# Optimization experiments

Measured on AMD Instinct MI355X. Metric: run time of the kernel, lower is better.

Reference implementation:

```python
import jax, jax.numpy as jnp
import numpy as np

B, S, HID, NH, HD, E, K = 8, 1024, 1024, 16, 64, 8, 2
IDIM = 2 * HD  # expert internal dim
EPS = 1e-5


def layer_norm(x, g, b):
    m = jnp.mean(x, axis=-1, keepdims=True)
    v = jnp.mean(jnp.square(x - m), axis=-1, keepdims=True)
    return (x - m) * jax.lax.rsqrt(v + EPS) * g + b


def setup_inputs() -> dict:
    key = jax.random.key(0)
    ks = jax.random.split(key, 12)
    n = jax.random.normal
    return {
        "queries": n(ks[0], (B, S, HID), jnp.float32),
        "keys": n(ks[1], (B, S, HID), jnp.float32),
        "values": n(ks[2], (B, S, HID), jnp.float32),
        "memorys": n(ks[3], (B, NH, S, HD), jnp.float32),
        "Wq": n(ks[4], (HD, HD), jnp.float32) * 0.02,
        "Wk": n(ks[5], (HD, HD), jnp.float32) * 0.02,
        "Wv": n(ks[6], (HD, HD), jnp.float32) * 0.02,
        "forget_gate": n(ks[7], (HD,), jnp.float32),
        "gate_W": n(ks[8], (E, HD), jnp.float32) * 0.02,
        "gate_b": jnp.zeros((E,), jnp.float32),
        "ln1_g": jnp.ones((E, HD), jnp.float32),
        "ln1_b": jnp.zeros((E, HD), jnp.float32),
        "W1": n(ks[9], (E, IDIM, HD), jnp.float32) * 0.02,
        "ln2_g": jnp.ones((E, IDIM), jnp.float32),
        "ln2_b": jnp.zeros((E, IDIM), jnp.float32),
        "W2": n(ks[10], (E, HD, IDIM), jnp.float32) * 0.02,
        "b2": jnp.zeros((E, HD), jnp.float32),
    }


def reference(queries, keys, values, memorys, Wq, Wk, Wv, forget_gate,
              gate_W, gate_b, ln1_g, ln1_b, W1, ln2_g, ln2_b, W2, b2):
    bsz, seq, _ = queries.shape
    gelu = lambda x: jax.nn.gelu(x, approximate=False)

    # head split: [B,S,HID] -> [B,NH,S,HD]
    q = queries.reshape(bsz, seq, NH, HD).transpose(0, 2, 1, 3)
    k = keys.reshape(bsz, seq, NH, HD).transpose(0, 2, 1, 3)
    v = values.reshape(bsz, seq, NH, HD).transpose(0, 2, 1, 3)

    q_ = q @ Wq.T
    k_ = k @ Wk.T
    v_ = v @ Wv.T

    # gated memory cell
    cell = k_ * v_ + forget_gate * memorys
    current_memorys = (1.0 - forget_gate) * cell + forget_gate * memorys
    cell_values = q_ * current_memorys  # [B,NH,S,HD]

    # token-mixing MoE (per-token, over last dim)
    x = cell_values.reshape(-1, HD)  # [N, HD], N = B*NH*S
    logits = x @ gate_W.T + gate_b  # [N, E]
    topv, topi = jax.lax.top_k(logits, K)  # [N, K]
    # sparse combine weights [N, E] (raw gate values, as in the original)
    w = jnp.sum(jax.nn.one_hot(topi, E, dtype=x.dtype) * topv[..., None], axis=1)

    def expert_fwd(g1, b1, w1, g2, b2_, w2, bias2):
        h = gelu(layer_norm(x, g1, b1)) @ w1.T      # [N, IDIM]
        h = gelu(layer_norm(h, g2, b2_)) @ w2.T + bias2  # [N, HD]
        return h

    all_out = jax.vmap(expert_fwd)(ln1_g, ln1_b, W1, ln2_g, ln2_b, W2, b2)  # [E,N,HD]
    moe = jnp.einsum('ne,end->nd', w, all_out)  # [N, HD]

    token_mixing = moe.reshape(bsz, NH, seq, HD).transpose(0, 2, 1, 3).reshape(bsz, seq, NH * HD)
    return token_mixing, current_memorys
```

## Files before the change

### kernel.cpp

```cpp
#include <hip/hip_runtime.h>
#include <stdint.h>

typedef unsigned short u16;
typedef unsigned int   u32;
typedef unsigned long long u64;
typedef __attribute__((ext_vector_type(8))) short short8;
typedef __attribute__((ext_vector_type(4))) short s16x4;
typedef __attribute__((ext_vector_type(4))) float f32x4;

#define B_    8
#define S_    1024
#define HID_  1024
#define NH_   16
#define HD_   64
#define E_    8
#define IDIM_ 128
#define NTOK  (B_*NH_*S_)

#define CSTRIDE 16

__device__ __forceinline__ float bf2f(u16 u){ return __uint_as_float(((u32)u) << 16); }
__device__ __forceinline__ u16 f2bf(float f){
    u32 u = __float_as_uint(f);
    u32 r = u + 0x7fffu + ((u >> 16) & 1u);
    return (u16)(r >> 16);
}
__device__ __forceinline__ short8 frag8(const float* __restrict__ p){
    float4 a = *(const float4*)p;
    float4 b = *(const float4*)(p + 4);
    short8 r;
    r[0]=(short)f2bf(a.x); r[1]=(short)f2bf(a.y); r[2]=(short)f2bf(a.z); r[3]=(short)f2bf(a.w);
    r[4]=(short)f2bf(b.x); r[5]=(short)f2bf(b.y); r[6]=(short)f2bf(b.z); r[7]=(short)f2bf(b.w);
    return r;
}
__device__ __forceinline__ float gelu_exact(float x){
    return 0.5f * x * (1.0f + erff(x * 0.70710678118654752f));
}
__device__ __forceinline__ float gelu_f(float x){
    float z = 1.5957691216057308f * (x + 0.044715f * x * x * x);
    float e = __expf(z);
    float t = 1.0f - 2.0f / (e + 1.0f);
    return 0.5f * x * (1.0f + t);
}

__global__ void k_zero(u32* c){
    c[threadIdx.x] = 0;
}

__global__ __launch_bounds__(256) void k_prep(
    const float* __restrict__ W1, const float* __restrict__ W2,
    u16* __restrict__ wB1, u16* __restrict__ wB2)
{
    const int i = blockIdx.x*256 + threadIdx.x;
    wB1[i] = f2bf(W1[i]);
    wB2[i] = f2bf(W2[i]);
}

__global__ __launch_bounds__(256,2) void k_mem(
    const float* __restrict__ kin, const float* __restrict__ vin, const float* __restrict__ mem,
    const float* __restrict__ Wk,  const float* __restrict__ Wv,  const float* __restrict__ fg,
    float* __restrict__ cur_out)
{
    const int lane = threadIdx.x & 63;
    const int wid  = threadIdx.x >> 6;
    const int m    = lane & 15;
    const int kg   = lane >> 4;

    const int slab  = blockIdx.x;
    const int chunk = slab & 3, h = (slab >> 2) & 15, b = slab >> 6;
    const int tw    = chunk*256 + wid*64;

    const float* kbase = kin + ((size_t)b*S_)*HID_ + h*64;
    const float* vbase = vin + ((size_t)b*S_)*HID_ + h*64;

    f32x4 accK[4][4], accV[4][4];
    const f32x4 z = {0.f,0.f,0.f,0.f};
    #pragma unroll
    for (int i=0;i<4;i++){ accK[i][0]=z;accK[i][1]=z;accK[i][2]=z;accK[i][3]=z;
                           accV[i][0]=z;accV[i][1]=z;accV[i][2]=z;accV[i][3]=z; }

    #pragma unroll
    for (int kk=0; kk<2; kk++){
        const int k0 = kk*32 + kg*8;
        short8 aF[4], bF[4];
        #pragma unroll
        for (int mt=0; mt<4; mt++) aF[mt] = frag8(kbase + (size_t)(tw + mt*16 + m)*HID_ + k0);
        #pragma unroll
        for (int ct=0; ct<4; ct++) bF[ct] = frag8(Wk + (ct*16 + m)*64 + k0);
        #pragma unroll
        for (int mt=0; mt<4; mt++)
            #pragma unroll
            for (int ct=0; ct<4; ct++)
                accK[mt][ct] = __builtin_amdgcn_mfma_f32_16x16x32_bf16(aF[mt], bF[ct], accK[mt][ct], 0,0,0);
    }
    #pragma unroll
    for (int kk=0; kk<2; kk++){
        const int k0 = kk*32 + kg*8;
        short8 aF[4], bF[4];
        #pragma unroll
        for (int mt=0; mt<4; mt++) aF[mt] = frag8(vbase + (size_t)(tw + mt*16 + m)*HID_ + k0);
        #pragma unroll
        for (int ct=0; ct<4; ct++) bF[ct] = frag8(Wv + (ct*16 + m)*64 + k0);
        #pragma unroll
        for (int mt=0; mt<4; mt++)
            #pragma unroll
            for (int ct=0; ct<4; ct++)
                accV[mt][ct] = __builtin_amdgcn_mfma_f32_16x16x32_bf16(aF[mt], bF[ct], accV[mt][ct], 0,0,0);
    }

    const size_t nb = ((size_t)(b*NH_ + h)) << 10;
    float fgv[4];
    #pragma unroll
    for (int ct=0; ct<4; ct++) fgv[ct] = fg[ct*16 + m];

    #pragma unroll
    for (int mt=0; mt<4; mt++){
        #pragma unroll
        for (int r=0; r<4; r++){
            const int tok = tw + mt*16 + kg*4 + r;
            const size_t rowo = (nb + (size_t)tok)*64;
            #pragma unroll
            for (int ct=0; ct<4; ct++){
                const int d = ct*16 + m;
                const float kd = accK[mt][ct][r];
                const float vd = accV[mt][ct][r];
                const float f  = fgv[ct];
                const float mv = mem[rowo + d];
                const float cell = kd*vd + f*mv;
                cur_out[rowo + d] = (1.0f - f)*cell + f*mv;
            }
        }
    }
}

__global__ __launch_bounds__(256,2) void k_q(
    const float* __restrict__ qin, const float* __restrict__ cur_in, const float* __restrict__ Wq,
    float* __restrict__ out0)
{
    const int lane = threadIdx.x & 63;
    const int wid  = threadIdx.x >> 6;
    const int m    = lane & 15;
    const int kg   = lane >> 4;

    const int slab  = blockIdx.x;
    const int chunk = slab & 3, h = (slab >> 2) & 15, b = slab >> 6;
    const int tw    = chunk*256 + wid*64;

    const float* qbase = qin + ((size_t)b*S_)*HID_ + h*64;

    f32x4 accQ[4][4];
    const f32x4 z = {0.f,0.f,0.f,0.f};
    #pragma unroll
    for (int i=0;i<4;i++){ accQ[i][0]=z;accQ[i][1]=z;accQ[i][2]=z;accQ[i][3]=z; }

    #pragma unroll
    for (int kk=0; kk<2; kk++){
        const int k0 = kk*32 + kg*8;
        short8 aF[4], bF[4];
        #pragma unroll
        for (int mt=0; mt<4; mt++) aF[mt] = frag8(qbase + (size_t)(tw + mt*16 + m)*HID_ + k0);
        #pragma unroll
        for (int ct=0; ct<4; ct++) bF[ct] = frag8(Wq + (ct*16 + m)*64 + k0);
        #pragma unroll
        for (int mt=0; mt<4; mt++)
            #pragma unroll
            for (int ct=0; ct<4; ct++)
                accQ[mt][ct] = __builtin_amdgcn_mfma_f32_16x16x32_bf16(aF[mt], bF[ct], accQ[mt][ct], 0,0,0);
    }

    const size_t nb = ((size_t)(b*NH_ + h)) << 10;
    #pragma unroll
    for (int mt=0; mt<4; mt++){
        #pragma unroll
        for (int r=0; r<4; r++){
            const int tok = tw + mt*16 + kg*4 + r;
            const size_t curo = (nb + (size_t)tok)*64;
            const size_t po   = ((size_t)(b*S_ + tok)*NH_ + h)*64;
            #pragma unroll
            for (int ct=0; ct<4; ct++){
                const int d = ct*16 + m;
                out0[po + d] = accQ[mt][ct][r] * cur_in[curo + d];
            }
        }
    }
}

__global__ __launch_bounds__(256,2) void k_gate(
    const float* __restrict__ x_src, const float* __restrict__ gW, const float* __restrict__ gB,
    uint4* __restrict__ topiv, u32* __restrict__ counts)
{
    __shared__ float sGW[512], sGB[8];
    __shared__ u32 sWc[4][8];
    const int tid = threadIdx.x;
    for (int i = tid; i < 512; i += 256) sGW[i] = gW[i];
    if (tid < 8) sGB[tid] = gB[tid];
    __syncthreads();

    const int n = blockIdx.x*256 + tid;
    const int s = n & (S_-1), h = (n >> 10) & (NH_-1), b = n >> 14;
    const size_t po = ((size_t)(b*S_ + s)*NH_ + h)*64;

    float lg[8];
    #pragma unroll
    for (int e = 0; e < 8; e++) lg[e] = sGB[e];

    for (int dc = 0; dc < 16; dc++){
        float4 x4 = ((const float4*)(x_src + po))[dc];
        float xv[4] = {x4.x, x4.y, x4.z, x4.w};
        #pragma unroll
        for (int i = 0; i < 4; i++){
            const int d = dc*4 + i;
            #pragma unroll
            for (int e = 0; e < 8; e++) lg[e] += sGW[e*64 + d] * xv[i];
        }
    }

    int i1 = 0; float v1 = lg[0];
    #pragma unroll
    for (int e = 1; e < 8; e++){ if (lg[e] > v1){ v1 = lg[e]; i1 = e; } }
    int i2 = -1; float v2 = -3.0e38f;
    #pragma unroll
    for (int e = 0; e < 8; e++){ if (e != i1 && lg[e] > v2){ v2 = lg[e]; i2 = e; } }

    topiv[n] = make_uint4((u32)i1, (u32)i2, __float_as_uint(v1), __float_as_uint(v2));

    const int lane = tid & 63;
    const int w    = tid >> 6;
    #pragma unroll
    for (int e = 0; e < 8; e++){
        u64 m1 = __ballot(i1 == e);
        u64 m2 = __ballot(i2 == e);
        if (lane == 0) sWc[w][e] = (u32)(__popcll(m1) + __popcll(m2));
    }
    __syncthreads();
    if (tid < 8){
        u32 t = sWc[0][tid] + sWc[1][tid] + sWc[2][tid] + sWc[3][tid];
        if (t) atomicAdd(&counts[tid*CSTRIDE], t);
    }
}

__global__ __launch_bounds__(256,2) void k_scatter(
    const uint4* __restrict__ topiv, const u32* __restrict__ counts, u32* __restrict__ cursors,
    u32* __restrict__ bucket, int2* __restrict__ slots)
{
    __shared__ u32 sC1[4][8], sC2[4][8];
    __shared__ u32 sB1[4][8], sB2w[4][8];

    const int tid = threadIdx.x;
    const int n = blockIdx.x*256 + tid;
    uint4 t = topiv[n];
    const int i1 = (int)t.x, i2 = (int)t.y;

    int off[8]; int acc = 0;
    #pragma unroll
    for (int e = 0; e < 8; e++){ off[e] = acc; acc += (int)counts[e*CSTRIDE]; }

    const int s = n & (S_-1), h = (n >> 10) & (NH_-1), b = n >> 14;
    const u32 pos32 = (u32)((b*S_ + s)*NH_ + h);

    const int lane = tid & 63;
    const int w    = tid >> 6;
    const u64 low = (1ull << lane) - 1ull;

    u64 myM1 = 0, myM2 = 0;
    #pragma unroll
    for (int e = 0; e < 8; e++){
        u64 m1 = __ballot(i1 == e);
        u64 m2 = __ballot(i2 == e);
        if (i1 == e) myM1 = m1;
        if (i2 == e) myM2 = m2;
        if (lane == 0){ sC1[w][e] = (u32)__popcll(m1); sC2[w][e] = (u32)__popcll(m2); }
    }
    __syncthreads();

    if (tid < 8){
        const int e = tid;
        u32 tot = 0;
        #pragma unroll
        for (int ww = 0; ww < 4; ww++) tot += sC1[ww][e] + sC2[ww][e];
        u32 base = tot ? atomicAdd(&cursors[e*CSTRIDE], tot) : 0;
        u32 run = base;
        #pragma unroll
        for (int ww = 0; ww < 4; ww++){
            sB1[ww][e] = run; run += sC1[ww][e];
            sB2w[ww][e] = run; run += sC2[ww][e];
        }
    }
    __syncthreads();

    const int slot1 = off[i1] + (int)sB1[w][i1] + (int)__popcll(myM1 & low);
    const int slot2 = off[i2] + (int)sB2w[w][i2] + (int)__popcll(myM2 & low);

    bucket[slot1] = pos32;
    bucket[slot2] = pos32;
    slots[n] = make_int2(slot1, slot2);
}

__global__ __launch_bounds__(256,3) void k_expert_mfma(
    const float* __restrict__ x_src, const u32* __restrict__ bucket, const u32* __restrict__ counts,
    const u16* __restrict__ wB1, const u16* __restrict__ wB2,
    const float* __restrict__ l1g, const float* __restrict__ l1b,
    const float* __restrict__ l2g, const float* __restrict__ l2b,
    const float* __restrict__ b2,  u16* __restrict__ aout)
{
    const int e = blockIdx.x >> 10;
    const int c = blockIdx.x & 1023;
    const int cnt = (int)counts[e*CSTRIDE];
    const int aBase = c * 128;
    if (aBase >= cnt) return;

    int off = 0;
    #pragma unroll
    for (int ee = 0; ee < 8; ee++){ if (ee < e) off += (int)counts[ee*CSTRIDE]; }

    __shared__ __align__(16) u16 sH[4][32*128];
    __shared__ float sL1g[64], sL1b[64], sL2g[128], sL2b[128], sB2[64];

    const int tid = threadIdx.x;
    if (tid < 64){ sL1g[tid] = l1g[e*64+tid]; sL1b[tid] = l1b[e*64+tid]; sB2[tid] = b2[e*64+tid]; }
    else if (tid < 192){ int t = tid - 64; sL2g[t] = l2g[e*128+t]; sL2b[t] = l2b[e*128+t]; }
    __syncthreads();

    const int lane = tid & 63;
    const int w    = tid >> 6;
    const int m    = lane & 15;
    const int kg   = lane >> 4;
    const int tb   = aBase + w*32;
    char* sHw = (char*)(&sH[w][0]);

    int pos[2];
    #pragma unroll
    for (int t = 0; t < 2; t++){
        int a = tb + t*16 + m; if (a > cnt-1) a = cnt-1;
        pos[t] = (int)bucket[off + a];
    }

    short8 aF[2][2];
    #pragma unroll
    for (int t = 0; t < 2; t++){
        const float* rp = x_src + ((size_t)(u32)pos[t] << 6);
        float4 v0 = *(const float4*)(rp + kg*8);
        float4 v1 = *(const float4*)(rp + kg*8 + 4);
        float4 v2 = *(const float4*)(rp + 32 + kg*8);
        float4 v3 = *(const float4*)(rp + 32 + kg*8 + 4);
        float s0 = (v0.x+v0.y+v0.z+v0.w) + (v1.x+v1.y+v1.z+v1.w)
                 + (v2.x+v2.y+v2.z+v2.w) + (v3.x+v3.y+v3.z+v3.w);
        float s1 = (v0.x*v0.x+v0.y*v0.y+v0.z*v0.z+v0.w*v0.w)
                 + (v1.x*v1.x+v1.y*v1.y+v1.z*v1.z+v1.w*v1.w)
                 + (v2.x*v2.x+v2.y*v2.y+v2.z*v2.z+v2.w*v2.w)
                 + (v3.x*v3.x+v3.y*v3.y+v3.z*v3.z+v3.w*v3.w);
        s0 += __shfl_xor(s0, 16); s0 += __shfl_xor(s0, 32);
        s1 += __shfl_xor(s1, 16); s1 += __shfl_xor(s1, 32);
        const float mu = s0 * (1.0f/64.0f);
        const float rs = rsqrtf(s1 * (1.0f/64.0f) - mu*mu + 1e-5f);
        float xv[16] = {v0.x,v0.y,v0.z,v0.w, v1.x,v1.y,v1.z,v1.w,
                        v2.x,v2.y,v2.z,v2.w, v3.x,v3.y,v3.z,v3.w};
        #pragma unroll
        for (int kk = 0; kk < 2; kk++){
            short8 f;
            #pragma unroll
            for (int j = 0; j < 8; j++){
                const int k = kk*32 + kg*8 + j;
                f[j] = (short)f2bf(gelu_f((xv[kk*8+j] - mu)*rs*sL1g[k] + sL1b[k]));
            }
            aF[t][kk] = f;
        }
    }

    const f32x4 z = {0.f,0.f,0.f,0.f};
    f32x4 acc1[2][8];
    #pragma unroll
    for (int t = 0; t < 2; t++)
        #pragma unroll
        for (int ct = 0; ct < 8; ct++) acc1[t][ct] = z;

    const u16* wB1e = wB1 + e*8192;
    #pragma unroll
    for (int kk = 0; kk < 2; kk++){
        const int k0 = kk*32 + kg*8;
        short8 bF[8];
        #pragma unroll
        for (int ct = 0; ct < 8; ct++)
            bF[ct] = *(const short8*)(wB1e + (ct*16 + m)*64 + k0);
        #pragma unroll
        for (int t = 0; t < 2; t++)
            #pragma unroll
            for (int ct = 0; ct < 8; ct++)
                acc1[t][ct] = __builtin_amdgcn_mfma_f32_16x16x32_bf16(aF[t][kk], bF[ct], acc1[t][ct], 0,0,0);
    }

    #pragma unroll
    for (int t = 0; t < 2; t++){
        #pragma unroll
        for (int r = 0; r < 4; r++){
            float p0 = 0.f, p1 = 0.f;
            #pragma unroll
            for (int ct = 0; ct < 8; ct++){ float v = acc1[t][ct][r]; p0 += v; p1 += v*v; }
            #pragma unroll
            for (int msk = 1; msk < 16; msk <<= 1){
                p0 += __shfl_xor(p0, msk);
                p1 += __shfl_xor(p1, msk);
            }
            const float mu = p0 * (1.0f/128.0f);
            const float rs = rsqrtf(p1 * (1.0f/128.0f) - mu*mu + 1e-5f);
            const int row = t*16 + kg*4 + r;
            #pragma unroll
            for (int ct = 0; ct < 8; ct++){
                const int col = ct*16 + m;
                *(u16*)(sHw + (((row<<8) + (col<<1)) ^ ((row&7)<<4)))
                    = f2bf(gelu_f((acc1[t][ct][r] - mu)*rs*sL2g[col] + sL2b[col]));
            }
        }
    }

    f32x4 acc2[2][4];
    #pragma unroll
    for (int t = 0; t < 2; t++)
        #pragma unroll
        for (int ct = 0; ct < 4; ct++) acc2[t][ct] = z;

    const u16* wB2e = wB2 + e*8192;
    #pragma unroll
    for (int kk = 0; kk < 4; kk++){
        const int k0 = kk*32 + kg*8;
        short8 aF2[2], bF2[4];
        #pragma unroll
        for (int t = 0; t < 2; t++){
            const int row = t*16 + m;
            aF2[t] = *(const short8*)(sHw + (((row<<8) + (k0<<1)) ^ ((row&7)<<4)));
        }
        #pragma unroll
        for (int ct = 0; ct < 4; ct++)
            bF2[ct] = *(const short8*)(wB2e + (ct*16 + m)*128 + k0);
        #pragma unroll
        for (int t = 0; t < 2; t++)
            #pragma unroll
            for (int ct = 0; ct < 4; ct++)
                acc2[t][ct] = __builtin_amdgcn_mfma_f32_16x16x32_bf16(aF2[t], bF2[ct], acc2[t][ct], 0,0,0);
    }

    #pragma unroll
    for (int t = 0; t < 2; t++){
        #pragma unroll
        for (int r = 0; r < 4; r++){
            const int row = t*16 + kg*4 + r;
            #pragma unroll
            for (int ct = 0; ct < 4; ct++){
                const int col = ct*16 + m;
                *(u16*)(sHw + (((row<<7) + (col<<1)) ^ ((row&7)<<4)))
                    = f2bf(acc2[t][ct][r] + sB2[col]);
            }
        }
    }

    #pragma unroll
    for (int it = 0; it < 4; it++){
        const int idx = it*64 + lane;
        const int row = idx >> 3, qq = idx & 7;
        if (tb + row < cnt){
            uint4 v = *(const uint4*)(sHw + (((row<<7) + (qq<<4)) ^ ((row&7)<<4)));
            *(uint4*)(aout + ((size_t)(off + tb + row) << 6) + qq*8) = v;
        }
    }
}

__global__ __launch_bounds__(256,2) void k_expert(
    const float* __restrict__ x_src, const u32* __restrict__ bucket, const u32* __restrict__ counts,
    const float* __restrict__ W1,  const float* __restrict__ W2,
    const float* __restrict__ l1g, const float* __restrict__ l1b,
    const float* __restrict__ l2g, const float* __restrict__ l2b,
    const float* __restrict__ b2,  u16* __restrict__ aout)
{
    const int e = blockIdx.x >> 9;
    const int c = blockIdx.x & 511;
    const int cnt = (int)counts[e*CSTRIDE];
    const int aBase = c * 256;
    if (aBase >= cnt) return;

    int off = 0;
    for (int ee = 0; ee < 8; ee++){ if (ee < e) off += (int)counts[ee*CSTRIDE]; }

    __shared__ float sW1[8192];
    __shared__ float sW2T[128*68];
    __shared__ float sL1g[64], sL1b[64], sL2g[128], sL2b[128], sB2[64];
    const int tid = threadIdx.x;
    for (int i = tid; i < 8192; i += 256){
        sW1[i] = W1[e*8192 + i];
        int d = i >> 7, j = i & 127;
        sW2T[j*68 + d] = W2[e*8192 + i];
    }
    if (tid < 64){ sL1g[tid] = l1g[e*64+tid]; sL1b[tid] = l1b[e*64+tid]; sB2[tid] = b2[e*64+tid]; }
    if (tid < 128){ sL2g[tid] = l2g[e*128+tid]; sL2b[tid] = l2b[e*128+tid]; }
    __syncthreads();

    const int a = aBase + tid;
    if (a >= cnt) return;
    const u32 pos32 = bucket[off + a];

    float g[64];
    #pragma unroll
    for (int i = 0; i < 16; i++){
        float4 t = ((const float4*)(x_src + (size_t)pos32*64))[i];
        g[i*4+0]=t.x; g[i*4+1]=t.y; g[i*4+2]=t.z; g[i*4+3]=t.w;
    }

    float s0 = 0.f, s1 = 0.f;
    #pragma unroll
    for (int d = 0; d < 64; d++){ s0 += g[d]; s1 += g[d]*g[d]; }
    float m  = s0 * (1.0f/64.0f);
    float va = s1 * (1.0f/64.0f) - m*m;
    float rs = rsqrtf(va + 1e-5f);
    #pragma unroll
    for (int d = 0; d < 64; d++) g[d] = gelu_exact((g[d]-m)*rs*sL1g[d] + sL1b[d]);

    u32 hpk[64];
    float hs = 0.f, hs2 = 0.f;
    for (int jp = 0; jp < 64; jp++){
        float h0, h1;
        {
            float a0=0.f,a1=0.f,a2=0.f,a3=0.f;
            const float4* w4 = (const float4*)&sW1[(2*jp)*64];
            #pragma unroll
            for (int i = 0; i < 16; i++){
                float4 ww = w4[i];
                a0 += ww.x*g[i*4+0]; a1 += ww.y*g[i*4+1]; a2 += ww.z*g[i*4+2]; a3 += ww.w*g[i*4+3];
            }
            h0 = (a0+a1)+(a2+a3);
        }
        {
            float a0=0.f,a1=0.f,a2=0.f,a3=0.f;
            const float4* w4 = (const float4*)&sW1[(2*jp+1)*64];
            #pragma unroll
            for (int i = 0; i < 16; i++){
                float4 ww = w4[i];
                a0 += ww.x*g[i*4+0]; a1 += ww.y*g[i*4+1]; a2 += ww.z*g[i*4+2]; a3 += ww.w*g[i*4+3];
            }
            h1 = (a0+a1)+(a2+a3);
        }
        hs += h0 + h1; hs2 += h0*h0 + h1*h1;
        hpk[jp] = (u32)f2bf(h0) | ((u32)f2bf(h1) << 16);
    }
    float m2  = hs  * (1.0f/128.0f);
    float va2 = hs2 * (1.0f/128.0f) - m2*m2;
    float rs2 = rsqrtf(va2 + 1e-5f);

    float acc[64];
    #pragma unroll
    for (int d = 0; d < 64; d++) acc[d] = sB2[d];
    for (int j = 0; j < 128; j++){
        float hj = bf2f((u16)((j & 1) ? (hpk[j>>1] >> 16) : (hpk[j>>1] & 0xffffu)));
        float gh = gelu_exact((hj - m2)*rs2*sL2g[j] + sL2b[j]);
        const float4* w2t = (const float4*)&sW2T[j*68];
        #pragma unroll
        for (int d4 = 0; d4 < 16; d4++){
            float4 w = w2t[d4];
            acc[d4*4+0] += gh * w.x;
            acc[d4*4+1] += gh * w.y;
            acc[d4*4+2] += gh * w.z;
            acc[d4*4+3] += gh * w.w;
        }
    }

    u16* op = aout + (size_t)(off + a) * 64;
    #pragma unroll
    for (int dc = 0; dc < 8; dc++){
        uint4 o;
        o.x = (u32)f2bf(acc[dc*8+0]) | ((u32)f2bf(acc[dc*8+1]) << 16);
        o.y = (u32)f2bf(acc[dc*8+2]) | ((u32)f2bf(acc[dc*8+3]) << 16);
        o.z = (u32)f2bf(acc[dc*8+4]) | ((u32)f2bf(acc[dc*8+5]) << 16);
        o.w = (u32)f2bf(acc[dc*8+6]) | ((u32)f2bf(acc[dc*8+7]) << 16);
        ((uint4*)op)[dc] = o;
    }
}

__global__ __launch_bounds__(256,4) void k_combine(
    const u16* __restrict__ aout, const uint4* __restrict__ topiv,
    const int2* __restrict__ slots, float* __restrict__ out0)
{
    const int tid = threadIdx.x;
    const int p   = blockIdx.x*16 + (tid >> 4);
    const int cq  = tid & 15;

    const int h  = p & (NH_-1);
    const int bs = p >> 4;
    const int b  = bs >> 10, s = bs & (S_-1);
    const int n  = ((b*NH_ + h) << 10) + s;

    uint4 t = topiv[n];
    float w1 = __uint_as_float(t.z), w2 = __uint_as_float(t.w);
    int2 sl = slots[n];

    uint2 ua = *(const uint2*)(aout + (size_t)sl.x*64 + cq*4);
    uint2 ub = *(const uint2*)(aout + (size_t)sl.y*64 + cq*4);

    float4 o;
    o.x = w1*bf2f((u16)(ua.x & 0xffffu)) + w2*bf2f((u16)(ub.x & 0xffffu));
    o.y = w1*bf2f((u16)(ua.x >> 16))     + w2*bf2f((u16)(ub.x >> 16));
    o.z = w1*bf2f((u16)(ua.y & 0xffffu)) + w2*bf2f((u16)(ub.y & 0xffffu));
    o.w = w1*bf2f((u16)(ua.y >> 16))     + w2*bf2f((u16)(ub.y >> 16));
    *(float4*)(out0 + (size_t)p*64 + cq*4) = o;
}

extern "C" void kernel_launch(void* const* d_in, const int* in_sizes, int n_in,
                              void* d_out, int out_size, void* d_ws, size_t ws_size,
                              hipStream_t stream)
{
    const float* qin = (const float*)d_in[0];
    const float* kin = (const float*)d_in[1];
    const float* vin = (const float*)d_in[2];
    const float* mem = (const float*)d_in[3];
    const float* Wq  = (const float*)d_in[4];
    const float* Wk  = (const float*)d_in[5];
    const float* Wv  = (const float*)d_in[6];
    const float* fg  = (const float*)d_in[7];
    const float* gW  = (const float*)d_in[8];
    const float* gB  = (const float*)d_in[9];
    const float* l1g = (const float*)d_in[10];
    const float* l1b = (const float*)d_in[11];
    const float* W1  = (const float*)d_in[12];
    const float* l2g = (const float*)d_in[13];
    const float* l2b = (const float*)d_in[14];
    const float* W2  = (const float*)d_in[15];
    const float* b2  = (const float*)d_in[16];

    float* out0 = (float*)d_out;
    float* out1 = out0 + (size_t)NTOK * 64;

    char* ws = (char*)d_ws;
    u16*   aout   = (u16*)(ws);
    uint4* topiv  = (uint4*)(ws + (size_t)33554432);
    int2*  slots  = (int2*)(ws + (size_t)35651584);
    u32*   bucket = (u32*)(ws + (size_t)36700160);
    u32*   counts = (u32*)(ws + (size_t)37748736);
    u32*   cursors = (u32*)(ws + (size_t)37749248);
    u16*   wB1    = (u16*)(ws + (size_t)37749760);
    u16*   wB2    = (u16*)(ws + (size_t)37880832);
    const size_t WS_NEED = 38011904;

    (void)in_sizes; (void)n_in; (void)out_size;

    const bool use_mfma = (ws_size >= WS_NEED);

    k_zero   <<<1, 256, 0, stream>>>(counts);
    if (use_mfma)
        k_prep <<<256, 256, 0, stream>>>(W1, W2, wB1, wB2);
    k_mem    <<<512, 256, 0, stream>>>(kin, vin, mem, Wk, Wv, fg, out1);
    k_q      <<<512, 256, 0, stream>>>(qin, out1, Wq, out0);
    k_gate   <<<NTOK/256, 256, 0, stream>>>(out0, gW, gB, topiv, counts);
    k_scatter<<<NTOK/256, 256, 0, stream>>>(topiv, counts, cursors, bucket, slots);
    if (use_mfma)
        k_expert_mfma<<<E_*1024, 256, 0, stream>>>(out0, bucket, counts, wB1, wB2,
                                                   l1g, l1b, l2g, l2b, b2, aout);
    else
        k_expert <<<E_*512, 256, 0, stream>>>(out0, bucket, counts, W1, W2,
                                              l1g, l1b, l2g, l2b, b2, aout);
    k_combine<<<NTOK/16, 256, 0, stream>>>(aout, topiv, slots, out0);
}
```

Before: 326.9 us.

## Precompute per-expert LN1+GELU bf16 rows in gate kernel, reuse out0 buffer

The gate kernel now also computes LayerNorm1 and GELU for each token's two selected experts and writes them as bf16 in place over the fp32 out0 row (two 64-wide bf16 halves fill the same bytes). Bucket entries encode which half to read, so the MFMA expert kernel loads ready bf16 operands and skips per-slot LN1/GELU work; its launch bounds rise to 4 blocks per SU. This removes duplicated normalization work and halves expert input read bytes, but it overwrites out0 before combine. Combine writes out0 afterwards, so that is likely fine. The fallback k_expert path would still read fp32, but writeXg is off in that case.

```diff
diff --git a/kernel.cpp b/kernel.cpp
--- a/kernel.cpp
+++ b/kernel.cpp
@@ -186,26 +186,34 @@
 }
 
 __global__ __launch_bounds__(256,2) void k_gate(
-    const float* __restrict__ x_src, const float* __restrict__ gW, const float* __restrict__ gB,
-    uint4* __restrict__ topiv, u32* __restrict__ counts)
-{
-    __shared__ float sGW[512], sGB[8];
+    float* __restrict__ x_io, const float* __restrict__ gW, const float* __restrict__ gB,
+    const float* __restrict__ l1g, const float* __restrict__ l1b,
+    uint4* __restrict__ topiv, u32* __restrict__ counts, int writeXg)
+{
+    __shared__ float sGW[512], sGB[8], sG1[512], sB1g[512];
     __shared__ u32 sWc[4][8];
     const int tid = threadIdx.x;
-    for (int i = tid; i < 512; i += 256) sGW[i] = gW[i];
+    for (int i = tid; i < 512; i += 256){ sGW[i] = gW[i]; sG1[i] = l1g[i]; sB1g[i] = l1b[i]; }
     if (tid < 8) sGB[tid] = gB[tid];
     __syncthreads();
 
     const int n = blockIdx.x*256 + tid;
     const int s = n & (S_-1), h = (n >> 10) & (NH_-1), b = n >> 14;
-    const size_t po = ((size_t)(b*S_ + s)*NH_ + h)*64;
-
+    const int pos = (b*S_ + s)*NH_ + h;
+    float* rowp = x_io + ((size_t)pos << 6);
+
+    float xr[64];
     float lg[8];
     #pragma unroll
     for (int e = 0; e < 8; e++) lg[e] = sGB[e];
-
+    float s0 = 0.f, s1 = 0.f;
+
+    #pragma unroll
     for (int dc = 0; dc < 16; dc++){
-        float4 x4 = ((const float4*)(x_src + po))[dc];
+        float4 x4 = ((const float4*)rowp)[dc];
+        xr[dc*4+0]=x4.x; xr[dc*4+1]=x4.y; xr[dc*4+2]=x4.z; xr[dc*4+3]=x4.w;
+        s0 += x4.x + x4.y + x4.z + x4.w;
+        s1 += x4.x*x4.x + x4.y*x4.y + x4.z*x4.z + x4.w*x4.w;
         float xv[4] = {x4.x, x4.y, x4.z, x4.w};
         #pragma unroll
         for (int i = 0; i < 4; i++){
@@ -223,6 +231,34 @@
     for (int e = 0; e < 8; e++){ if (e != i1 && lg[e] > v2){ v2 = lg[e]; i2 = e; } }
 
     topiv[n] = make_uint4((u32)i1, (u32)i2, __float_as_uint(v1), __float_as_uint(v2));
+
+    if (writeXg){
+        const float mu = s0 * (1.0f/64.0f);
+        const float rs = rsqrtf(s1 * (1.0f/64.0f) - mu*mu + 1e-5f);
+        u16* xgrow = (u16*)x_io + ((size_t)pos << 7);
+        #pragma unroll
+        for (int half = 0; half < 2; half++){
+            const int ee = half ? i2 : i1;
+            const float* g1 = &sG1[ee*64];
+            const float* b1 = &sB1g[ee*64];
+            uint4* dst = (uint4*)(xgrow + half*64);
+            #pragma unroll
+            for (int dc = 0; dc < 8; dc++){
+                float vv[8];
+                #pragma unroll
+                for (int j = 0; j < 8; j++){
+                    const int d = dc*8 + j;
+                    vv[j] = gelu_f((xr[d] - mu)*rs*g1[d] + b1[d]);
+                }
+                uint4 o;
+                o.x = (u32)f2bf(vv[0]) | ((u32)f2bf(vv[1]) << 16);
+                o.y = (u32)f2bf(vv[2]) | ((u32)f2bf(vv[3]) << 16);
+                o.z = (u32)f2bf(vv[4]) | ((u32)f2bf(vv[5]) << 16);
+                o.w = (u32)f2bf(vv[6]) | ((u32)f2bf(vv[7]) << 16);
+                dst[dc] = o;
+            }
+        }
+    }
 
     const int lane = tid & 63;
     const int w    = tid >> 6;
@@ -291,15 +327,14 @@
     const int slot1 = off[i1] + (int)sB1[w][i1] + (int)__popcll(myM1 & low);
     const int slot2 = off[i2] + (int)sB2w[w][i2] + (int)__popcll(myM2 & low);
 
-    bucket[slot1] = pos32;
-    bucket[slot2] = pos32;
+    bucket[slot1] = (pos32 << 1);
+    bucket[slot2] = (pos32 << 1) | 1u;
     slots[n] = make_int2(slot1, slot2);
 }
 
-__global__ __launch_bounds__(256,3) void k_expert_mfma(
+__global__ __launch_bounds__(256,4) void k_expert_mfma(
     const float* __restrict__ x_src, const u32* __restrict__ bucket, const u32* __restrict__ counts,
     const u16* __restrict__ wB1, const u16* __restrict__ wB2,
-    const float* __restrict__ l1g, const float* __restrict__ l1b,
     const float* __restrict__ l2g, const float* __restrict__ l2b,
     const float* __restrict__ b2,  u16* __restrict__ aout)
 {
@@ -314,11 +349,11 @@
     for (int ee = 0; ee < 8; ee++){ if (ee < e) off += (int)counts[ee*CSTRIDE]; }
 
     __shared__ __align__(16) u16 sH[4][32*128];
-    __shared__ float sL1g[64], sL1b[64], sL2g[128], sL2b[128], sB2[64];
+    __shared__ float sL2g[128], sL2b[128], sB2[64];
 
     const int tid = threadIdx.x;
-    if (tid < 64){ sL1g[tid] = l1g[e*64+tid]; sL1b[tid] = l1b[e*64+tid]; sB2[tid] = b2[e*64+tid]; }
-    else if (tid < 192){ int t = tid - 64; sL2g[t] = l2g[e*128+t]; sL2b[t] = l2b[e*128+t]; }
+    if (tid < 128){ sL2g[tid] = l2g[e*128+tid]; sL2b[tid] = l2b[e*128+tid]; }
+    else if (tid < 192){ sB2[tid-128] = b2[e*64 + tid-128]; }
     __syncthreads();
 
     const int lane = tid & 63;
@@ -328,43 +363,15 @@
     const int tb   = aBase + w*32;
     char* sHw = (char*)(&sH[w][0]);
 
-    int pos[2];
+    const u16* xg = (const u16*)x_src;
+    short8 aF[2][2];
     #pragma unroll
     for (int t = 0; t < 2; t++){
         int a = tb + t*16 + m; if (a > cnt-1) a = cnt-1;
-        pos[t] = (int)bucket[off + a];
-    }
-
-    short8 aF[2][2];
-    #pragma unroll
-    for (int t = 0; t < 2; t++){
-        const float* rp = x_src + ((size_t)(u32)pos[t] << 6);
-        float4 v0 = *(const float4*)(rp + kg*8);
-        float4 v1 = *(const float4*)(rp + kg*8 + 4);
-        float4 v2 = *(const float4*)(rp + 32 + kg*8);
-        float4 v3 = *(const float4*)(rp + 32 + kg*8 + 4);
-        float s0 = (v0.x+v0.y+v0.z+v0.w) + (v1.x+v1.y+v1.z+v1.w)
-                 + (v2.x+v2.y+v2.z+v2.w) + (v3.x+v3.y+v3.z+v3.w);
-        float s1 = (v0.x*v0.x+v0.y*v0.y+v0.z*v0.z+v0.w*v0.w)
-                 + (v1.x*v1.x+v1.y*v1.y+v1.z*v1.z+v1.w*v1.w)
-                 + (v2.x*v2.x+v2.y*v2.y+v2.z*v2.z+v2.w*v2.w)
-                 + (v3.x*v3.x+v3.y*v3.y+v3.z*v3.z+v3.w*v3.w);
-        s0 += __shfl_xor(s0, 16); s0 += __shfl_xor(s0, 32);
-        s1 += __shfl_xor(s1, 16); s1 += __shfl_xor(s1, 32);
-        const float mu = s0 * (1.0f/64.0f);
-        const float rs = rsqrtf(s1 * (1.0f/64.0f) - mu*mu + 1e-5f);
-        float xv[16] = {v0.x,v0.y,v0.z,v0.w, v1.x,v1.y,v1.z,v1.w,
-                        v2.x,v2.y,v2.z,v2.w, v3.x,v3.y,v3.z,v3.w};
-        #pragma unroll
-        for (int kk = 0; kk < 2; kk++){
-            short8 f;
-            #pragma unroll
-            for (int j = 0; j < 8; j++){
-                const int k = kk*32 + kg*8 + j;
-                f[j] = (short)f2bf(gelu_f((xv[kk*8+j] - mu)*rs*sL1g[k] + sL1b[k]));
-            }
-            aF[t][kk] = f;
-        }
+        const u32 bv = bucket[off + a];
+        const u16* rp = xg + (((size_t)(bv >> 1)) << 7) + (bv & 1u)*64;
+        aF[t][0] = *(const short8*)(rp + kg*8);
+        aF[t][1] = *(const short8*)(rp + 32 + kg*8);
     }
 
     const f32x4 z = {0.f,0.f,0.f,0.f};
@@ -495,7 +502,7 @@
 
     const int a = aBase + tid;
     if (a >= cnt) return;
-    const u32 pos32 = bucket[off + a];
+    const u32 pos32 = bucket[off + a] >> 1;
 
     float g[64];
     #pragma unroll
@@ -646,11 +653,12 @@
         k_prep <<<256, 256, 0, stream>>>(W1, W2, wB1, wB2);
     k_mem    <<<512, 256, 0, stream>>>(kin, vin, mem, Wk, Wv, fg, out1);
     k_q      <<<512, 256, 0, stream>>>(qin, out1, Wq, out0);
-    k_gate   <<<NTOK/256, 256, 0, stream>>>(out0, gW, gB, topiv, counts);
+    k_gate   <<<NTOK/256, 256, 0, stream>>>(out0, gW, gB, l1g, l1b, topiv, counts,
+                                            use_mfma ? 1 : 0);
     k_scatter<<<NTOK/256, 256, 0, stream>>>(topiv, counts, cursors, bucket, slots);
     if (use_mfma)
         k_expert_mfma<<<E_*1024, 256, 0, stream>>>(out0, bucket, counts, wB1, wB2,
-                                                   l1g, l1b, l2g, l2b, b2, aout);
+                                                   l2g, l2b, b2, aout);
     else
         k_expert <<<E_*512, 256, 0, stream>>>(out0, bucket, counts, W1, W2,
                                               l1g, l1b, l2g, l2b, b2, aout);
```

New measurement: 328.4 us. About the same (+0.5%).
